# Kernel optimization log

Hardware: AMD Instinct MI355X
Metric: run time of the kernel (lower is better)

## Reference

```python
import jax, jax.numpy as jnp
import numpy as np

S, B, I, H = 512, 64, 512, 512

def setup_inputs() -> dict:
    key = jax.random.key(0)
    ks = jax.random.split(key, 10)
    inp = {
        'x':    jax.random.normal(ks[0], (S, B, I), dtype=jnp.float32),
        'W_xi': jax.random.normal(ks[1], (H, I), dtype=jnp.float32) * (1.0 / np.sqrt(I)),
        'W_hi': jax.random.normal(ks[2], (H, H), dtype=jnp.float32) * (1.0 / np.sqrt(H)),
        'b_i':  jax.random.normal(ks[3], (H,), dtype=jnp.float32),
        'W_xc': jax.random.normal(ks[4], (H, I), dtype=jnp.float32) * (1.0 / np.sqrt(I)),
        'W_hc': jax.random.normal(ks[5], (H, H), dtype=jnp.float32) * (1.0 / np.sqrt(H)),
        'b_c':  jax.random.normal(ks[6], (H,), dtype=jnp.float32),
        'W_xo': jax.random.normal(ks[7], (H, I), dtype=jnp.float32) * (1.0 / np.sqrt(I)),
        'W_ho': jax.random.normal(ks[8], (H, H), dtype=jnp.float32) * (1.0 / np.sqrt(H)),
        'b_o':  jax.random.normal(ks[9], (H,), dtype=jnp.float32),
    }
    return inp

def reference(x, W_xi, W_hi, b_i, W_xc, W_hc, b_c, W_xo, W_ho, b_o):
    seq_len, batch, _ = x.shape
    hidden = W_hi.shape[0]
    # Precompute all input-to-gate projections in one pass: [S,B,H] each
    xi = jnp.einsum('sbi,hi->sbh', x, W_xi)
    xc = jnp.einsum('sbi,hi->sbh', x, W_xc)
    xo = jnp.einsum('sbi,hi->sbh', x, W_xo)

    h0 = jnp.zeros((batch, hidden), dtype=x.dtype)
    c0 = jnp.zeros((batch, hidden), dtype=x.dtype)

    def step(carry, xs):
        h, c = carry
        xi_t, xc_t, xo_t = xs
        i_t = jax.nn.sigmoid(xi_t + h @ W_hi.T + b_i)
        c_hat = jnp.tanh(xc_t + h @ W_hc.T + b_c)
        c = (1.0 - i_t) * c + i_t * c_hat  # coupled forget gate f = 1 - i
        o_t = jax.nn.sigmoid(xo_t + h @ W_ho.T + b_o)
        h = o_t * jnp.tanh(c)
        return (h, c), h

    (h_t, c_t), output = jax.lax.scan(step, (h0, c0), (xi, xc, xo))
    # output: [S,B,H] (time-major, matching torch after transposes)
    return output, h_t, c_t
```

## Files before the change

kernel.cpp:

```cpp
#include <hip/hip_runtime.h>
#include <math.h>

#define SEQ   512
#define BATCH 64
#define HID   512
#define NROW  1536
#define XROW_FLOATS ((size_t)SEQ * NROW * BATCH)
#define HBUF_QWORDS (2 * BATCH * HID)
#define SBH ((size_t)SEQ * BATCH * HID)

__device__ __forceinline__ float sigf(float x) {
    return 1.f / (1.f + __expf(-x));
}
__device__ __forceinline__ float tanh_fast(float x) {
    float ax = fabsf(x);
    float e = __expf(-2.f * ax);
    float r = (1.f - e) / (1.f + e);
    return copysignf(r, x);
}
template <int CTRL>
__device__ __forceinline__ float dpp_add(float v) {
    int x = __builtin_amdgcn_update_dpp(0, __builtin_bit_cast(int, v),
                                        CTRL, 0xf, 0xf, true);
    return v + __builtin_bit_cast(float, x);
}

__global__ __launch_bounds__(256) void xproj_kernel(
    const float* __restrict__ x, const float* __restrict__ Wxi,
    const float* __restrict__ Wxc, const float* __restrict__ Wxo,
    float* __restrict__ xrow)
{
    extern __shared__ float lds[];
    float* xT = lds;
    const int tid = threadIdx.x, lane = tid & 63, wv = tid >> 6;
    float* wl = lds + 256 * 65 + wv * (8 * 256);
    const int t = blockIdx.x;

    for (int kh = 0; kh < 2; ++kh) {
        __syncthreads();
        for (int b = wv; b < 64; b += 4) {
            const float* xp = x + ((size_t)t * 64 + b) * 512 + kh * 256;
            #pragma unroll
            for (int q = 0; q < 4; ++q) {
                int k = lane + q * 64;
                xT[k * 65 + b] = xp[k];
            }
        }
        __syncthreads();

        for (int m = 0; m < 48; ++m) {
            const int Bk = wv + 4 * m;
            const int R0 = Bk * 8;
            #pragma unroll
            for (int r = 0; r < 8; ++r) {
                const int R = R0 + r, g = R >> 9, j = R & 511;
                const float* wsrc = (g == 0) ? Wxi : ((g == 1) ? Wxc : Wxo);
                const float4 w4 = *(const float4*)(wsrc + (size_t)j * 512 + kh * 256 + lane * 4);
                *(float4*)(wl + r * 256 + lane * 4) = w4;
            }
            float acc[8] = {0.f, 0.f, 0.f, 0.f, 0.f, 0.f, 0.f, 0.f};
            #pragma unroll 2
            for (int c = 0; c < 64; ++c) {
                const float x0 = xT[(4 * c + 0) * 65 + lane];
                const float x1 = xT[(4 * c + 1) * 65 + lane];
                const float x2 = xT[(4 * c + 2) * 65 + lane];
                const float x3 = xT[(4 * c + 3) * 65 + lane];
                #pragma unroll
                for (int r = 0; r < 8; ++r) {
                    const float4 w4 = *(const float4*)(wl + r * 256 + c * 4);
                    acc[r] += x0 * w4.x + x1 * w4.y + x2 * w4.z + x3 * w4.w;
                }
            }
            #pragma unroll
            for (int r = 0; r < 8; ++r) {
                const size_t o = ((size_t)t * NROW + R0 + r) * 64 + lane;
                if (kh) xrow[o] += acc[r];
                else    xrow[o]  = acc[r];
            }
        }
    }
}

#define HPAD 10
#define H_FLOATS (512 * HPAD)
__global__ __launch_bounds__(512, 2) void scan_kernel(
    const float* __restrict__ xrow,
    const float* __restrict__ Whi, const float* __restrict__ Whc, const float* __restrict__ Who,
    const float* __restrict__ bi, const float* __restrict__ bc, const float* __restrict__ bo,
    unsigned long long* __restrict__ hbuf, float* __restrict__ out)
{
    extern __shared__ float lds[];
    float* hlds = lds;
    float* gbuf = lds + H_FLOATS;
    float* biasL = gbuf + 384;

    const int tid = threadIdx.x, lane = tid & 63;
    const int gid = blockIdx.x & 7;
    const int m   = blockIdx.x >> 3;
    const int rg  = tid >> 5, ks = tid & 31;

    float w3r[16][3];
    #pragma unroll
    for (int r = 0; r < 3; ++r) {
        const int rho = rg * 3 + r;
        const int g = rho >> 4, jloc = rho & 15;
        const float* wsrc = (g == 0) ? Whi : ((g == 1) ? Whc : Who);
        const float* wp = wsrc + (size_t)(m * 16 + jloc) * 512 + ks;
        #pragma unroll
        for (int i = 0; i < 16; ++i) w3r[i][r] = wp[32 * i];
    }
    if (tid < 48) {
        const int g = tid >> 4, jloc = tid & 15;
        const float* bb = (g == 0) ? bi : ((g == 1) ? bc : bo);
        biasL[tid] = bb[m * 16 + jloc];
    }

    const int ejl = tid & 15, eb = tid >> 4;
    const int jg  = m * 16 + ejl;
    const int bg  = gid * 8 + eb;
    float creg = 0.f;

    if (tid < 128) hlds[jg * HPAD + eb] = 0.f;
    __syncthreads();

    const bool own_k = ((tid >> 4) == m);

    for (int t = 0; t < SEQ; ++t) {
        float xr0 = 0.f, xr1 = 0.f, xr2 = 0.f;
        if (tid < 128) {
            const size_t base = ((size_t)t * NROW + jg) * 64 + bg;
            xr0 = xrow[base];
            xr1 = xrow[base + (size_t)512 * 64];
            xr2 = xrow[base + (size_t)1024 * 64];
        }

        if (!own_k) {
            const unsigned long long* hsrc =
                hbuf + (size_t)(t & 1) * (BATCH * HID) + (size_t)gid * 8 * 512 + tid;
            const unsigned tgt = (unsigned)t;
            unsigned long long hv[8];
            #pragma unroll
            for (int q = 0; q < 8; ++q)
                hv[q] = __hip_atomic_load(hsrc + (size_t)q * 512, __ATOMIC_RELAXED,
                                          __HIP_MEMORY_SCOPE_AGENT);
            unsigned pend = 0xffu;
            while (pend) {
                unsigned np = 0;
                #pragma unroll
                for (int q = 0; q < 8; ++q) {
                    if ((pend >> q) & 1) {
                        if ((unsigned)(hv[q] >> 32) >= tgt) {
                            hlds[tid * HPAD + q] =
                                __builtin_bit_cast(float, (unsigned)hv[q]);
                        } else np |= 1u << q;
                    }
                }
                if (np) {
                    #pragma unroll
                    for (int q = 0; q < 8; ++q)
                        if ((np >> q) & 1)
                            hv[q] = __hip_atomic_load(hsrc + (size_t)q * 512,
                                                      __ATOMIC_RELAXED,
                                                      __HIP_MEMORY_SCOPE_AGENT);
                    __builtin_amdgcn_s_sleep(1);
                }
                pend = np;
            }
        }
        __syncthreads();

        float acc[3][8];
        #pragma unroll
        for (int r = 0; r < 3; ++r)
            #pragma unroll
            for (int b = 0; b < 8; ++b) acc[r][b] = 0.f;

        {
            const float* hb = hlds + ks * HPAD;
            #pragma unroll
            for (int i = 0; i < 16; ++i) {
                float hv2[8];
                *(float2*)&hv2[0] = *(const float2*)(hb + i * (32 * HPAD) + 0);
                *(float2*)&hv2[2] = *(const float2*)(hb + i * (32 * HPAD) + 2);
                *(float2*)&hv2[4] = *(const float2*)(hb + i * (32 * HPAD) + 4);
                *(float2*)&hv2[6] = *(const float2*)(hb + i * (32 * HPAD) + 6);
                #pragma unroll
                for (int r = 0; r < 3; ++r)
                    #pragma unroll
                    for (int b = 0; b < 8; ++b)
                        acc[r][b] += w3r[i][r] * hv2[b];
            }
            #pragma unroll
            for (int r = 0; r < 3; ++r)
                #pragma unroll
                for (int b = 0; b < 8; ++b) {
                    float v = acc[r][b];
                    v = dpp_add<0x121>(v);
                    v = dpp_add<0x122>(v);
                    v = dpp_add<0x124>(v);
                    v = dpp_add<0x128>(v);
                    v = dpp_add<0x142>(v);
                    acc[r][b] = v;
                }
            if (lane == 16 || lane == 48) {
                #pragma unroll
                for (int r = 0; r < 3; ++r) {
                    float* gp = gbuf + (rg * 3 + r) * 8;
                    *(float4*)gp       = make_float4(acc[r][0], acc[r][1], acc[r][2], acc[r][3]);
                    *(float4*)(gp + 4) = make_float4(acc[r][4], acc[r][5], acc[r][6], acc[r][7]);
                }
            }
        }
        __syncthreads();

        if (tid < 128) {
            const float pi = xr0 + biasL[ejl]      + gbuf[(0 * 16 + ejl) * 8 + eb];
            const float pc = xr1 + biasL[16 + ejl] + gbuf[(1 * 16 + ejl) * 8 + eb];
            const float po = xr2 + biasL[32 + ejl] + gbuf[(2 * 16 + ejl) * 8 + eb];
            const float it = sigf(pi);
            const float ch = tanh_fast(pc);
            const float ot = sigf(po);
            creg = (1.f - it) * creg + it * ch;
            const float hn = ot * tanh_fast(creg);
            const unsigned long long pv =
                ((unsigned long long)(unsigned)(t + 1) << 32) |
                (unsigned long long)__builtin_bit_cast(unsigned, hn);
            __hip_atomic_store(hbuf + (size_t)((t + 1) & 1) * (BATCH * HID)
                                    + (size_t)bg * 512 + jg,
                               pv, __ATOMIC_RELAXED, __HIP_MEMORY_SCOPE_AGENT);
            hlds[jg * HPAD + eb] = hn;
            out[((size_t)t * 64 + bg) * 512 + jg] = hn;
            if (t == SEQ - 1) {
                out[SBH + (size_t)bg * 512 + jg] = hn;
                out[SBH + 32768 + (size_t)bg * 512 + jg] = creg;
            }
        }
    }
}

extern "C" void kernel_launch(void* const* d_in, const int* in_sizes, int n_in,
                              void* d_out, int out_size, void* d_ws, size_t ws_size,
                              hipStream_t stream)
{
    const float* x   = (const float*)d_in[0];
    const float* Wxi = (const float*)d_in[1];
    const float* Whi = (const float*)d_in[2];
    const float* bi  = (const float*)d_in[3];
    const float* Wxc = (const float*)d_in[4];
    const float* Whc = (const float*)d_in[5];
    const float* bc  = (const float*)d_in[6];
    const float* Wxo = (const float*)d_in[7];
    const float* Who = (const float*)d_in[8];
    const float* bo  = (const float*)d_in[9];
    float* out = (float*)d_out;
    char* ws = (char*)d_ws;

    float*              xrow = (float*)ws;
    unsigned long long* hbuf = (unsigned long long*)(ws + XROW_FLOATS * 4);

    (void)hipMemsetAsync(hbuf, 0, (size_t)HBUF_QWORDS * 8, stream);

    hipLaunchKernelGGL(xproj_kernel, dim3(512), dim3(256), 99328, stream,
                       x, Wxi, Wxc, Wxo, xrow);
    hipLaunchKernelGGL(scan_kernel, dim3(256), dim3(512), 22208, stream,
                       xrow, Whi, Whc, Who, bi, bc, bo, hbuf, out);
}
```

Measured before the change: 4.856 ms.

## Rewrite input projection as register-tiled GEMM without shared memory

The x-projection kernel no longer stages a transposed x tile and weight rows in LDS. Each lane now computes an 8-row by 4-batch register tile, reading x and weights straight from global memory as float4 and writing float4 results. This removes the LDS footprint, the barriers and the split-K read-modify-write of the output, which should allow higher occupancy. In exchange it relies on L1/L2 caching for reuse of x and weights, and each lane's float4 weight loads are strided and uncoalesced.

```diff
diff --git a/kernel.cpp b/kernel.cpp
--- a/kernel.cpp
+++ b/kernel.cpp
@@ -30,54 +30,42 @@
     const float* __restrict__ Wxc, const float* __restrict__ Wxo,
     float* __restrict__ xrow)
 {
-    extern __shared__ float lds[];
-    float* xT = lds;
     const int tid = threadIdx.x, lane = tid & 63, wv = tid >> 6;
-    float* wl = lds + 256 * 65 + wv * (8 * 256);
     const int t = blockIdx.x;
-
-    for (int kh = 0; kh < 2; ++kh) {
-        __syncthreads();
-        for (int b = wv; b < 64; b += 4) {
-            const float* xp = x + ((size_t)t * 64 + b) * 512 + kh * 256;
-            #pragma unroll
-            for (int q = 0; q < 4; ++q) {
-                int k = lane + q * 64;
-                xT[k * 65 + b] = xp[k];
-            }
-        }
-        __syncthreads();
-
-        for (int m = 0; m < 48; ++m) {
-            const int Bk = wv + 4 * m;
-            const int R0 = Bk * 8;
+    const int bq = lane & 15;
+    const int rq = lane >> 4;
+    const float* xb = x + ((size_t)t * 64 + 4 * bq) * 512;
+
+    for (int mm = 0; mm < 12; ++mm) {
+        const int R0 = mm * 128 + wv * 32 + rq * 8;
+        const int g = R0 >> 9, j0 = R0 & 511;
+        const float* wsrc = (g == 0) ? Wxi : ((g == 1) ? Wxc : Wxo);
+        const float* wp = wsrc + (size_t)j0 * 512;
+
+        float acc[8][4];
+        #pragma unroll
+        for (int r = 0; r < 8; ++r)
+            #pragma unroll
+            for (int j = 0; j < 4; ++j) acc[r][j] = 0.f;
+
+        for (int k4 = 0; k4 < 128; ++k4) {
+            float4 xv[4];
+            #pragma unroll
+            for (int j = 0; j < 4; ++j)
+                xv[j] = *(const float4*)(xb + j * 512 + k4 * 4);
             #pragma unroll
             for (int r = 0; r < 8; ++r) {
-                const int R = R0 + r, g = R >> 9, j = R & 511;
-                const float* wsrc = (g == 0) ? Wxi : ((g == 1) ? Wxc : Wxo);
-                const float4 w4 = *(const float4*)(wsrc + (size_t)j * 512 + kh * 256 + lane * 4);
-                *(float4*)(wl + r * 256 + lane * 4) = w4;
-            }
-            float acc[8] = {0.f, 0.f, 0.f, 0.f, 0.f, 0.f, 0.f, 0.f};
-            #pragma unroll 2
-            for (int c = 0; c < 64; ++c) {
-                const float x0 = xT[(4 * c + 0) * 65 + lane];
-                const float x1 = xT[(4 * c + 1) * 65 + lane];
-                const float x2 = xT[(4 * c + 2) * 65 + lane];
-                const float x3 = xT[(4 * c + 3) * 65 + lane];
-                #pragma unroll
-                for (int r = 0; r < 8; ++r) {
-                    const float4 w4 = *(const float4*)(wl + r * 256 + c * 4);
-                    acc[r] += x0 * w4.x + x1 * w4.y + x2 * w4.z + x3 * w4.w;
-                }
-            }
-            #pragma unroll
-            for (int r = 0; r < 8; ++r) {
-                const size_t o = ((size_t)t * NROW + R0 + r) * 64 + lane;
-                if (kh) xrow[o] += acc[r];
-                else    xrow[o]  = acc[r];
-            }
-        }
+                const float4 w4 = *(const float4*)(wp + (size_t)r * 512 + k4 * 4);
+                #pragma unroll
+                for (int j = 0; j < 4; ++j)
+                    acc[r][j] += w4.x * xv[j].x + w4.y * xv[j].y
+                               + w4.z * xv[j].z + w4.w * xv[j].w;
+            }
+        }
+        #pragma unroll
+        for (int r = 0; r < 8; ++r)
+            *(float4*)(xrow + ((size_t)t * NROW + R0 + r) * 64 + 4 * bq) =
+                make_float4(acc[r][0], acc[r][1], acc[r][2], acc[r][3]);
     }
 }
 
@@ -260,7 +248,7 @@
 
     (void)hipMemsetAsync(hbuf, 0, (size_t)HBUF_QWORDS * 8, stream);
 
-    hipLaunchKernelGGL(xproj_kernel, dim3(512), dim3(256), 99328, stream,
+    hipLaunchKernelGGL(xproj_kernel, dim3(512), dim3(256), 0, stream,
                        x, Wxi, Wxc, Wxo, xrow);
     hipLaunchKernelGGL(scan_kernel, dim3(256), dim3(512), 22208, stream,
                        xrow, Whi, Whc, Who, bi, bc, bo, hbuf, out);
```

Measured after the change: 4.798 ms. About the same (-1.2%).
